# Optimization experiments

Hardware: AMD Instinct MI355X
Metric: run time of the kernel (lower is better)

Reference implementation:

```python
import jax, jax.numpy as jnp
import numpy as np
from jax import lax

NL, HID, DIN, DST, DCONV, DTR = 4, 256, 512, 16, 4, 16  # layers, d_model, expand*d_model, d_state, d_conv, dt_rank
B, H, W = 4, 256, 256


def setup_inputs() -> dict:
    key = jax.random.key(0)
    ks = jax.random.split(key, 8)
    def n(k, s, sc=0.02):
        return jax.random.normal(k, s, dtype=jnp.float32) * sc
    return {
        "x": jax.random.normal(ks[0], (B, 3, H, W), dtype=jnp.float32),
        "conv1_w": n(ks[1], (HID // 2, 3, 3, 3), 0.1), "conv1_b": jnp.zeros((HID // 2,), jnp.float32),
        "gn1_w": jnp.ones((HID // 2,), jnp.float32), "gn1_b": jnp.zeros((HID // 2,), jnp.float32),
        "conv2_w": n(ks[2], (HID, HID // 2, 3, 3), 0.05), "conv2_b": jnp.zeros((HID,), jnp.float32),
        "gn2_w": jnp.ones((HID,), jnp.float32), "gn2_b": jnp.zeros((HID,), jnp.float32),
        "ln_w": jnp.ones((NL, HID), jnp.float32), "ln_b": jnp.zeros((NL, HID), jnp.float32),
        "in_proj_w": n(ks[3], (NL, 2 * DIN, HID)),
        "conv1d_w": n(ks[4], (NL, DIN, 1, DCONV), 0.1), "conv1d_b": jnp.zeros((NL, DIN), jnp.float32),
        "x_proj_w": n(ks[5], (NL, DTR + 2 * DST, DIN)),
        "dt_proj_w": n(ks[6], (NL, DIN, DTR), 0.1),
        "dt_proj_b": jnp.full((NL, DIN), -4.6, dtype=jnp.float32),  # softplus(-4.6) ~ 0.01
        "A_log": jnp.broadcast_to(jnp.log(jnp.arange(1, DST + 1, dtype=jnp.float32)), (NL, DIN, DST)) + jnp.zeros((NL, DIN, DST), jnp.float32),
        "D": jnp.ones((NL, DIN), jnp.float32),
        "out_proj_w": n(ks[7], (NL, HID, DIN)),
    }


def conv2d_s2(x, w, b):
    y = lax.conv_general_dilated(x, w, (2, 2), [(1, 1), (1, 1)],
                                 dimension_numbers=('NCHW', 'OIHW', 'NCHW'))
    return y + b[None, :, None, None]


def group_norm(x, w, b, groups=8, eps=1e-5):
    Bb, C, Hh, Ww = x.shape
    xg = x.reshape(Bb, groups, C // groups, Hh, Ww)
    m = xg.mean((2, 3, 4), keepdims=True)
    v = xg.var((2, 3, 4), keepdims=True)
    xg = (xg - m) * lax.rsqrt(v + eps)
    return xg.reshape(Bb, C, Hh, Ww) * w[None, :, None, None] + b[None, :, None, None]


def layer_norm(x, w, b, eps=1e-5):
    m = x.mean(-1, keepdims=True)
    v = x.var(-1, keepdims=True)
    return (x - m) * lax.rsqrt(v + eps) * w + b


def mamba(x, ipw, cw, cb, xpw, dpw, dpb, A_log, Dp, opw):
    # x: [B, L, HID]
    Bb, L, _ = x.shape
    xz = jnp.einsum('bld,ed->ble', x, ipw)           # [B, L, 2*DIN]
    xc, z = jnp.split(xz, 2, axis=-1)
    # depthwise causal conv1d over L
    u = xc.transpose(0, 2, 1)                        # [B, DIN, L]
    u = lax.conv_general_dilated(u, cw, (1,), [(DCONV - 1, 0)],
                                 dimension_numbers=('NCH', 'OIH', 'NCH'),
                                 feature_group_count=DIN)
    xc = jax.nn.silu(u + cb[None, :, None]).transpose(0, 2, 1)  # [B, L, DIN]
    x_dbl = jnp.einsum('bld,ed->ble', xc, xpw)       # [B, L, DTR+2*DST]
    dt, Bm, Cm = jnp.split(x_dbl, [DTR, DTR + DST], axis=-1)
    delta = jax.nn.softplus(jnp.einsum('blr,dr->bld', dt, dpw) + dpb)  # [B, L, DIN]
    A = -jnp.exp(A_log)                              # [DIN, DST]
    dA = jnp.exp(jnp.einsum('bld,dn->bldn', delta, A))
    dBu = jnp.einsum('bld,bln,bld->bldn', delta, Bm, xc)

    def step(h, inp):
        dA_t, dBu_t, C_t = inp
        h = dA_t * h + dBu_t                         # [B, DIN, DST]
        return h, jnp.einsum('bdn,bn->bd', h, C_t)

    h0 = jnp.zeros((Bb, DIN, DST), x.dtype)
    _, ys = lax.scan(step, h0, (dA.transpose(1, 0, 2, 3), dBu.transpose(1, 0, 2, 3), Cm.transpose(1, 0, 2)))
    y = ys.transpose(1, 0, 2) + xc * Dp              # [B, L, DIN]
    y = y * jax.nn.silu(z)
    return jnp.einsum('bld,ed->ble', y, opw)         # [B, L, HID]


def reference(x, conv1_w, conv1_b, gn1_w, gn1_b, conv2_w, conv2_b, gn2_w, gn2_b,
              ln_w, ln_b, in_proj_w, conv1d_w, conv1d_b, x_proj_w, dt_proj_w,
              dt_proj_b, A_log, D, out_proj_w):
    y = jax.nn.silu(group_norm(conv2d_s2(x, conv1_w, conv1_b), gn1_w, gn1_b))
    y = jax.nn.silu(group_norm(conv2d_s2(y, conv2_w, conv2_b), gn2_w, gn2_b))
    Bb, C, h, w = y.shape
    s = y.reshape(Bb, C, h * w).transpose(0, 2, 1)   # b (h w) c
    for i in range(NL):
        s = s + mamba(layer_norm(s, ln_w[i], ln_b[i]), in_proj_w[i], conv1d_w[i],
                      conv1d_b[i], x_proj_w[i], dt_proj_w[i], dt_proj_b[i],
                      A_log[i], D[i], out_proj_w[i])
    return (s, h, w)
```

## Files before the change

### kernel.cpp

```cpp
#include <hip/hip_runtime.h>
#include <math.h>

#define BB 4
#define C1 128
#define H1 128
#define W1 128
#define C2 256
#define H2 64
#define W2 64
#define LSEQ 4096
#define HID 256
#define DIN 512
#define DST 16
#define DTR 16
#define NL 4
#define NCHUNK 64
#define LCH 64

typedef unsigned short u16;
using short8 = __attribute__((ext_vector_type(8))) short;
using f32x4  = __attribute__((ext_vector_type(4))) float;
using f32x2  = __attribute__((ext_vector_type(2))) float;

static __device__ __forceinline__ float dsilu(float x){
    return x / (1.0f + __expf(-x));
}
static __device__ __forceinline__ u16 f2bf(float f){
    unsigned u = __float_as_uint(f);
    u += 0x7FFF + ((u >> 16) & 1);
    return (u16)(u >> 16);
}
static __device__ __forceinline__ float bf2f(u16 v){
    return __uint_as_float(((unsigned)v) << 16);
}

#define GLL16(g, l) __builtin_amdgcn_global_load_lds( \
    (const __attribute__((address_space(1))) void*)(g), \
    (__attribute__((address_space(3))) void*)(l), 16, 0, 0)
#define GLL4(g, l) __builtin_amdgcn_global_load_lds( \
    (const __attribute__((address_space(1))) void*)(g), \
    (__attribute__((address_space(3))) void*)(l), 4, 0, 0)

#define VMW(n) asm volatile("s_waitcnt vmcnt(" #n ")" ::: "memory")

static __device__ __forceinline__ void blockbar(){
    asm volatile("" ::: "memory");
    __builtin_amdgcn_s_barrier();
    asm volatile("" ::: "memory");
}

__global__ void f2bf_kernel(const float* __restrict__ src, u16* __restrict__ dst){
    int idx = blockIdx.x * 256 + threadIdx.x;
    dst[idx] = f2bf(src[idx]);
}
__global__ void wdt_prep_kernel(const float* __restrict__ xpw, const float* __restrict__ dpw,
                                u16* __restrict__ wcomb){
    int idx = blockIdx.x * 256 + threadIdx.x;
    int k = idx & 511;
    int n = (idx >> 9) % 640;
    int layer = idx / (640*512);
    u16 val = 0;
    if(n < 512){
        const float* dp = dpw + ((long)layer*512 + n)*16;
        const float* xp = xpw + (long)layer*48*512 + k;
        float acc = 0.f;
        #pragma unroll
        for(int r = 0; r < 16; ++r) acc = fmaf(dp[r], xp[(long)r*512], acc);
        val = f2bf(acc);
    } else if(n < 544){
        int row = n - 512 + 16;
        val = f2bf(xpw[((long)layer*48 + row)*512 + k]);
    }
    wcomb[((long)layer*640 + n)*512 + k] = val;
}
__global__ void c2w_prep_kernel(const float* __restrict__ src, u16* __restrict__ dst){
    int idx = blockIdx.x * 256 + threadIdx.x;
    int ci = idx & 127, p = (idx >> 7) % 9, co = idx / (9*128);
    int kh = p / 3, kw = p - 3*kh;
    dst[idx] = f2bf(src[((co*128 + ci)*3 + kh)*3 + kw]);
}
__global__ void xt_border_kernel(unsigned* __restrict__ xt){
    int idx = blockIdx.x * 256 + threadIdx.x;
    int c2 = idx & 63;
    int cell = (idx >> 6) % 516;
    int b = idx / (516*64);
    int ih, iw;
    if(cell < 130){ ih = 0; iw = cell; }
    else if(cell < 260){ ih = 129; iw = cell - 130; }
    else if(cell < 388){ iw = 0; ih = cell - 259; }
    else { iw = 129; ih = cell - 387; }
    xt[((long)(b*130 + ih)*130 + iw)*64 + c2] = 0;
}

__global__ __launch_bounds__(256) void conv1_kernel(
        const float* __restrict__ x, const float* __restrict__ w,
        const float* __restrict__ bias, float* __restrict__ y){
    __shared__ float xs[9][260];
    int oh = blockIdx.x, b = blockIdx.y;
    int tid = threadIdx.x;
    #pragma unroll
    for(int r = 0; r < 9; ++r){
        int ci = r / 3, kh = r - 3*ci;
        int ih = 2*oh - 1 + kh;
        float v = 0.f;
        if(ih >= 0) v = x[((b*3 + ci)*256 + ih)*256 + tid];
        xs[r][tid + 1] = v;
        if(tid == 0) xs[r][0] = 0.f;
    }
    __syncthreads();
    int co = tid >> 1, h = tid & 1;
    float wr[27];
    #pragma unroll
    for(int j = 0; j < 27; ++j) wr[j] = w[co*27 + j];
    float bz = bias[co];
    long obase = ((long)((b*128 + co)*128 + oh))*128 + h*64;
    #pragma unroll 4
    for(int i = 0; i < 64; ++i){
        int iw0 = 2*(h*64 + i);
        float acc = bz;
        #pragma unroll
        for(int r = 0; r < 9; ++r){
            acc = fmaf(xs[r][iw0+0], wr[r*3+0], acc);
            acc = fmaf(xs[r][iw0+1], wr[r*3+1], acc);
            acc = fmaf(xs[r][iw0+2], wr[r*3+2], acc);
        }
        y[obase + i] = acc;
    }
}

__global__ void zero_stats_kernel(float* __restrict__ stats){
    stats[threadIdx.x] = 0.0f;
}

__global__ void gn_stats_kernel(const float* __restrict__ x, float* __restrict__ stats,
                                int elems_per_group){
    const int EPB = 16384;
    long base = (long)blockIdx.x * EPB;
    int g = (int)(base / elems_per_group);
    float s = 0.f, ss = 0.f;
    for(int j = threadIdx.x; j < EPB; j += 256){
        float v = x[base + j];
        s += v; ss += v*v;
    }
    #pragma unroll
    for(int off = 32; off; off >>= 1){
        s  += __shfl_down(s,  off);
        ss += __shfl_down(ss, off);
    }
    __shared__ float ls[4], lss[4];
    int wid = threadIdx.x >> 6, lane = threadIdx.x & 63;
    if(lane == 0){ ls[wid] = s; lss[wid] = ss; }
    __syncthreads();
    if(threadIdx.x == 0){
        atomicAdd(&stats[g],      ls[0]+ls[1]+ls[2]+ls[3]);
        atomicAdd(&stats[32+g], lss[0]+lss[1]+lss[2]+lss[3]);
    }
}

__global__ void gn1_transform_kernel(const float* __restrict__ y1, const float* __restrict__ stats,
                                     const float* __restrict__ w, const float* __restrict__ bias,
                                     u16* __restrict__ xt){
    __shared__ float tile[32][33];
    int b = blockIdx.z >> 7, ih = blockIdx.z & 127;
    int c0 = blockIdx.y * 32, w0 = blockIdx.x * 32;
    int tx = threadIdx.x, ty = threadIdx.y;
    const float cnt = 16.f * 128.f * 128.f;
    #pragma unroll
    for(int i = 0; i < 4; ++i){
        int ci = c0 + ty + i*8;
        int g = b*8 + (ci >> 4);
        float mean = stats[g] / cnt;
        float var  = stats[32+g] / cnt - mean*mean;
        float rstd = rsqrtf(var + 1e-5f);
        float v = y1[(((long)(b*C1 + ci))*H1 + ih)*W1 + w0 + tx];
        tile[ty + i*8][tx] = dsilu((v - mean) * rstd * w[ci] + bias[ci]);
    }
    __syncthreads();
    #pragma unroll
    for(int i = 0; i < 4; ++i){
        int iwl = ty + i*8;
        xt[((long)(b*130 + ih + 1)*130 + (w0 + iwl + 1))*128 + c0 + tx] = f2bf(tile[tx][iwl]);
    }
}

__global__ __launch_bounds__(256) void conv2gemm_bf16_kernel(
        const u16* __restrict__ xt, const u16* __restrict__ w2,
        const float* __restrict__ bias, float* __restrict__ y2t){
    __shared__ u16 Asm[3][64*32];
    __shared__ u16 Bsm[3][128*32];
    int m0 = blockIdx.x * 64, n0 = blockIdx.y * 128;
    int tid = threadIdx.x;
    long abase;
    {
        int r = tid >> 2;
        int kq = ((tid & 3) ^ ((r >> 1) & 3)) * 8;
        int m = m0 + r;
        int b = m >> 12, oh = (m >> 6) & 63, ow = m & 63;
        abase = ((long)(b*130 + 2*oh)*130 + 2*ow)*128 + kq;
    }
    int lda = tid*8;
    const u16* bbase[2]; int ldb[2];
    #pragma unroll
    for(int it = 0; it < 2; ++it){
        int c = it*256 + tid;
        int r = c >> 2;
        int kq = ((c & 3) ^ ((r >> 1) & 3)) * 8;
        bbase[it] = w2 + (long)(n0 + r)*1152 + kq;
        ldb[it] = c*8;
    }
    int wave = tid >> 6, lane = tid & 63;
    int wr = wave >> 1, wc = wave & 1;
    int lm = lane & 15, lq = lane >> 4;
    int swq = (lq ^ ((lm >> 1) & 3)) * 8;
    f32x4 acc[2][4] = {};
    #pragma unroll
    for(int pt = 0; pt < 2; ++pt){
        int p = pt >> 2, cs = pt & 3;
        int kh = p / 3, kw = p - 3*kh;
        int ao = (kh*130 + kw)*128 + cs*32;
        GLL16(xt + abase + ao, &Asm[pt][lda]);
        #pragma unroll
        for(int it = 0; it < 2; ++it)
            GLL16(bbase[it] + pt*32, &Bsm[pt][ldb[it]]);
    }
    for(int kk = 0; kk < 36; ++kk){
        int cur = kk % 3;
        if(kk + 2 < 36){
            int k2 = kk + 2;
            int nxt = (kk + 2) % 3;
            int p = k2 >> 2, cs = k2 & 3;
            int kh = p / 3, kw = p - 3*kh;
            int ao = (kh*130 + kw)*128 + cs*32;
            GLL16(xt + abase + ao, &Asm[nxt][lda]);
            #pragma unroll
            for(int it = 0; it < 2; ++it)
                GLL16(bbase[it] + k2*32, &Bsm[nxt][ldb[it]]);
            VMW(6);
        } else if(kk + 1 < 36){
            VMW(3);
        } else {
            VMW(0);
        }
        blockbar();
        short8 af[2], bf[4];
        #pragma unroll
        for(int i = 0; i < 2; ++i)
            af[i] = *(const short8*)&Asm[cur][(wr*32 + i*16 + lm)*32 + swq];
        #pragma unroll
        for(int j = 0; j < 4; ++j)
            bf[j] = *(const short8*)&Bsm[cur][(wc*64 + j*16 + lm)*32 + swq];
        #pragma unroll
        for(int i = 0; i < 2; ++i)
            #pragma unroll
            for(int j = 0; j < 4; ++j)
                acc[i][j] = __builtin_amdgcn_mfma_f32_16x16x32_bf16(af[i], bf[j], acc[i][j], 0, 0, 0);
        __builtin_amdgcn_sched_barrier(0);
        blockbar();
    }
    #pragma unroll
    for(int i = 0; i < 2; ++i){
        long row = m0 + wr*32 + i*16 + lq*4;
        #pragma unroll
        for(int j = 0; j < 4; ++j){
            int col = n0 + wc*64 + j*16 + lm;
            float bz = bias[col];
            #pragma unroll
            for(int r = 0; r < 4; ++r)
                y2t[(row + r)*256L + col] = acc[i][j][r] + bz;
        }
    }
}

__global__ void gn2t_stats_kernel(const float* __restrict__ y2t, float* __restrict__ stats){
    int b = blockIdx.y;
    long row0 = (long)b*LSEQ + blockIdx.x*64;
    int c = threadIdx.x;
    float s = 0.f, ss = 0.f;
    for(int r = 0; r < 64; ++r){
        float v = y2t[(row0 + r)*C2 + c];
        s += v; ss += v*v;
    }
    #pragma unroll
    for(int off = 16; off; off >>= 1){
        s  += __shfl_down(s,  off);
        ss += __shfl_down(ss, off);
    }
    if((c & 31) == 0){
        int g = b*8 + (c >> 5);
        atomicAdd(&stats[g], s);
        atomicAdd(&stats[32+g], ss);
    }
}

__global__ void gn2t_apply_ln_kernel(const float* __restrict__ y2t, const float* __restrict__ stats,
                                     const float* __restrict__ gw, const float* __restrict__ gb,
                                     const float* __restrict__ lw, const float* __restrict__ lb,
                                     float* __restrict__ s, u16* __restrict__ xln){
    long row = blockIdx.x;
    int c = threadIdx.x;
    int b = (int)(row >> 12);
    int g = b*8 + (c >> 5);
    const float cnt = 32.f * (float)LSEQ;
    float mean = stats[g] / cnt;
    float var  = stats[32+g] / cnt - mean*mean;
    float rstd = rsqrtf(var + 1e-5f);
    float v = dsilu((y2t[row*HID + c] - mean) * rstd * gw[c] + gb[c]);
    s[row*HID + c] = v;
    float sm = v, sq = v*v;
    #pragma unroll
    for(int off = 32; off; off >>= 1){
        sm += __shfl_down(sm, off);
        sq += __shfl_down(sq, off);
    }
    __shared__ float pa[4], pb[4], res[2];
    int wid = c >> 6, lane = c & 63;
    if(lane == 0){ pa[wid] = sm; pb[wid] = sq; }
    __syncthreads();
    if(c == 0){
        float t  = pa[0]+pa[1]+pa[2]+pa[3];
        float tt = pb[0]+pb[1]+pb[2]+pb[3];
        float m2 = t / 256.f;
        float v2 = tt / 256.f - m2*m2;
        res[0] = m2; res[1] = rsqrtf(v2 + 1e-5f);
    }
    __syncthreads();
    xln[row*HID + c] = f2bf((v - res[0]) * res[1] * lw[c] + lb[c]);
}

__global__ __launch_bounds__(256) void gemm_bf16_kernel(
        const u16* __restrict__ A, const u16* __restrict__ B, void* __restrict__ Cv,
        int K, int Nact, int ldc, int mode){
    __shared__ u16 Asm[3][128*32];
    __shared__ u16 Bsm[3][128*32];
    int m0 = blockIdx.x * 128, n0 = blockIdx.y * 128;
    int tid = threadIdx.x;
    int wave = tid >> 6, lane = tid & 63;
    int wr = wave >> 1, wc = wave & 1;
    int lm = lane & 15, lq = lane >> 4;
    int swq = (lq ^ ((lm >> 1) & 3)) * 8;
    const u16* ag[2]; const u16* bg[2]; int ldst[2];
    #pragma unroll
    for(int it = 0; it < 2; ++it){
        int c = it*256 + tid;
        int r = c >> 2;
        int kq = ((c & 3) ^ ((r >> 1) & 3)) * 8;
        ag[it] = A + (long)(m0 + r)*K + kq;
        bg[it] = B + (long)(n0 + r)*K + kq;
        ldst[it] = c*8;
    }
    f32x4 acc[4][4] = {};
    int nk = K >> 5;
    #pragma unroll
    for(int pt = 0; pt < 2; ++pt){
        int ko = pt << 5;
        #pragma unroll
        for(int it = 0; it < 2; ++it){
            GLL16(ag[it] + ko, &Asm[pt][ldst[it]]);
            GLL16(bg[it] + ko, &Bsm[pt][ldst[it]]);
        }
    }
    for(int kt = 0; kt < nk; ++kt){
        int cur = kt % 3;
        if(kt + 2 < nk){
            int nxt = (kt + 2) % 3;
            int ko = (kt + 2) << 5;
            #pragma unroll
            for(int it = 0; it < 2; ++it){
                GLL16(ag[it] + ko, &Asm[nxt][ldst[it]]);
                GLL16(bg[it] + ko, &Bsm[nxt][ldst[it]]);
            }
            VMW(8);
        } else if(kt + 1 < nk){
            VMW(4);
        } else {
            VMW(0);
        }
        blockbar();
        short8 af[4], bf[4];
        #pragma unroll
        for(int i = 0; i < 4; ++i){
            af[i] = *(const short8*)&Asm[cur][(wr*64 + i*16 + lm)*32 + swq];
            bf[i] = *(const short8*)&Bsm[cur][(wc*64 + i*16 + lm)*32 + swq];
        }
        #pragma unroll
        for(int i = 0; i < 4; ++i)
            #pragma unroll
            for(int j = 0; j < 4; ++j)
                acc[i][j] = __builtin_amdgcn_mfma_f32_16x16x32_bf16(af[i], bf[j], acc[i][j], 0, 0, 0);
        __builtin_amdgcn_sched_barrier(0);
        blockbar();
    }
    #pragma unroll
    for(int i = 0; i < 4; ++i){
        long row = m0 + wr*64 + i*16 + lq*4;
        #pragma unroll
        for(int j = 0; j < 4; ++j){
            int col = n0 + wc*64 + j*16 + lm;
            if(col < Nact){
                #pragma unroll
                for(int r = 0; r < 4; ++r){
                    long idx = (row + r)*(long)ldc + col;
                    if(mode == 2) ((u16*)Cv)[idx] = f2bf(acc[i][j][r]);
                    else          ((float*)Cv)[idx] = acc[i][j][r];
                }
            }
        }
    }
}

__global__ __launch_bounds__(256) void gemm_dtbc_kernel(
        const u16* __restrict__ A, const u16* __restrict__ B,
        const float* __restrict__ dpb, u16* __restrict__ dv,
        float* __restrict__ xdbl32){
    __shared__ u16 Asm[3][128*32];
    __shared__ u16 Bsm[3][128*32];
    int m0 = blockIdx.x * 128, n0 = blockIdx.y * 128;
    int tid = threadIdx.x;
    int wave = tid >> 6, lane = tid & 63;
    int wr = wave >> 1, wc = wave & 1;
    int lm = lane & 15, lq = lane >> 4;
    int swq = (lq ^ ((lm >> 1) & 3)) * 8;
    const u16* ag[2]; const u16* bg[2]; int ldst[2];
    #pragma unroll
    for(int it = 0; it < 2; ++it){
        int c = it*256 + tid;
        int r = c >> 2;
        int kq = ((c & 3) ^ ((r >> 1) & 3)) * 8;
        ag[it] = A + (long)(m0 + r)*512 + kq;
        bg[it] = B + (long)(n0 + r)*512 + kq;
        ldst[it] = c*8;
    }
    f32x4 acc[4][4] = {};
    #pragma unroll
    for(int pt = 0; pt < 2; ++pt){
        int ko = pt << 5;
        #pragma unroll
        for(int it = 0; it < 2; ++it){
            GLL16(ag[it] + ko, &Asm[pt][ldst[it]]);
            GLL16(bg[it] + ko, &Bsm[pt][ldst[it]]);
        }
    }
    for(int kt = 0; kt < 16; ++kt){
        int cur = kt % 3;
        if(kt + 2 < 16){
            int nxt = (kt + 2) % 3;
            int ko = (kt + 2) << 5;
            #pragma unroll
            for(int it = 0; it < 2; ++it){
                GLL16(ag[it] + ko, &Asm[nxt][ldst[it]]);
                GLL16(bg[it] + ko, &Bsm[nxt][ldst[it]]);
            }
            VMW(8);
        } else if(kt + 1 < 16){
            VMW(4);
        } else {
            VMW(0);
        }
        blockbar();
        short8 af[4], bf[4];
        #pragma unroll
        for(int i = 0; i < 4; ++i){
            af[i] = *(const short8*)&Asm[cur][(wr*64 + i*16 + lm)*32 + swq];
            bf[i] = *(const short8*)&Bsm[cur][(wc*64 + i*16 + lm)*32 + swq];
        }
        #pragma unroll
        for(int i = 0; i < 4; ++i)
            #pragma unroll
            for(int j = 0; j < 4; ++j)
                acc[i][j] = __builtin_amdgcn_mfma_f32_16x16x32_bf16(af[i], bf[j], acc[i][j], 0, 0, 0);
        __builtin_amdgcn_sched_barrier(0);
        blockbar();
    }
    if(n0 < 512){
        #pragma unroll
        for(int i = 0; i < 4; ++i){
            long row = m0 + wr*64 + i*16 + lq*4;
            #pragma unroll
            for(int j = 0; j < 4; ++j){
                int col = n0 + wc*64 + j*16 + lm;
                float bz = dpb[col];
                #pragma unroll
                for(int r = 0; r < 4; ++r){
                    float v = acc[i][j][r] + bz;
                    v = (v > 20.f) ? v : __logf(1.f + __expf(v));
                    dv[(row + r)*512L + col] = f2bf(v);
                }
            }
        }
    } else {
        #pragma unroll
        for(int i = 0; i < 4; ++i){
            long row = m0 + wr*64 + i*16 + lq*4;
            #pragma unroll
            for(int j = 0; j < 4; ++j){
                int lcol = wc*64 + j*16 + lm;
                if(lcol < 32){
                    #pragma unroll
                    for(int r = 0; r < 4; ++r)
                        xdbl32[(row + r)*32L + lcol] = acc[i][j][r];
                }
            }
        }
    }
}

__global__ __launch_bounds__(256) void gemm_out_ln_kernel(
        const u16* __restrict__ A, const u16* __restrict__ B,
        float* __restrict__ s, u16* __restrict__ xln,
        const float* __restrict__ lw, const float* __restrict__ lb){
    __shared__ u16 Asm[3][32*32];
    __shared__ u16 Bsm[3][256*32];
    __shared__ float lnred[2][2][16][2];
    int m0 = blockIdx.x * 32;
    int tid = threadIdx.x;
    int wave = tid >> 6, lane = tid & 63;
    int wr = wave >> 1, wc = wave & 1;
    int lm = lane & 15, lq = lane >> 4;
    int swq = (lq ^ ((lm >> 1) & 3)) * 8;
    const u16* agA[2]; int lda[2];
    #pragma unroll
    for(int it = 0; it < 2; ++it){
        int c = it*256 + tid;
// ... 47 lines not shown
        blockbar();
    }
    int row0 = m0 + wr*16 + lq*4;
    float psum[4] = {0.f,0.f,0.f,0.f}, psq[4] = {0.f,0.f,0.f,0.f};
    #pragma unroll
    for(int j = 0; j < 8; ++j){
        int col = wc*128 + j*16 + lm;
        #pragma unroll
        for(int r = 0; r < 4; ++r){
            long idx = (long)(row0 + r)*HID + col;
            float v = s[idx] + acc[j][r];
            acc[j][r] = v;
            s[idx] = v;
            psum[r] += v; psq[r] += v*v;
        }
    }
    #pragma unroll
    for(int mask = 1; mask <= 8; mask <<= 1){
        #pragma unroll
        for(int r = 0; r < 4; ++r){
            psum[r] += __shfl_xor(psum[r], mask);
            psq[r]  += __shfl_xor(psq[r],  mask);
        }
    }
    if(lm == 0){
        #pragma unroll
        for(int r = 0; r < 4; ++r){
            lnred[wr][wc][lq*4 + r][0] = psum[r];
            lnred[wr][wc][lq*4 + r][1] = psq[r];
        }
    }
    __syncthreads();
    float mean[4], rstd[4];
    #pragma unroll
    for(int r = 0; r < 4; ++r){
        float t  = lnred[wr][0][lq*4 + r][0] + lnred[wr][1][lq*4 + r][0];
        float tt = lnred[wr][0][lq*4 + r][1] + lnred[wr][1][lq*4 + r][1];
        mean[r] = t * (1.f/256.f);
        float var = tt * (1.f/256.f) - mean[r]*mean[r];
        rstd[r] = rsqrtf(var + 1e-5f);
    }
    #pragma unroll
    for(int j = 0; j < 8; ++j){
        int col = wc*128 + j*16 + lm;
        float wv = lw[col], bv = lb[col];
        #pragma unroll
        for(int r = 0; r < 4; ++r){
            long idx = (long)(row0 + r)*HID + col;
            xln[idx] = f2bf((acc[j][r] - mean[r]) * rstd[r] * wv + bv);
        }
    }
}

__global__ void conv1d_silu_kernel(const u16* __restrict__ xz, const float* __restrict__ w,
                                   const float* __restrict__ bias, u16* __restrict__ xcv){
    int idx = blockIdx.x * 256 + threadIdx.x;
    int e = idx * 8;
    int d0 = e & 511;
    long m = e >> 9;
    int l = (int)(m & 4095);
    short8 xrow[4];
    const u16* xp = xz + m*(2*DIN) + d0;
    #pragma unroll
    for(int j = 0; j < 4; ++j){
        int t = l - 3 + j;
        if(t >= 0) xrow[j] = *(const short8*)(xp + (long)(j-3)*(2*DIN));
        else       xrow[j] = (short8){0,0,0,0,0,0,0,0};
    }
    float wv[8][4];
    #pragma unroll
    for(int k = 0; k < 8; k += 2){
        float4 a = *(const float4*)(w + (d0+k)*4);
        float4 b = *(const float4*)(w + (d0+k+1)*4);
        wv[k][0]=a.x; wv[k][1]=a.y; wv[k][2]=a.z; wv[k][3]=a.w;
        wv[k+1][0]=b.x; wv[k+1][1]=b.y; wv[k+1][2]=b.z; wv[k+1][3]=b.w;
    }
    float bz[8];
    {
        float4 a = *(const float4*)(bias + d0);
        float4 b = *(const float4*)(bias + d0 + 4);
        bz[0]=a.x; bz[1]=a.y; bz[2]=a.z; bz[3]=a.w;
        bz[4]=b.x; bz[5]=b.y; bz[6]=b.z; bz[7]=b.w;
    }
    short8 out;
    #pragma unroll
    for(int k = 0; k < 8; ++k){
        float acc = bz[k];
        #pragma unroll
        for(int j = 0; j < 4; ++j)
            acc = fmaf(bf2f((u16)xrow[j][k]), wv[k][j], acc);
        out[k] = (short)f2bf(dsilu(acc));
    }
    *(short8*)(xcv + m*DIN + d0) = out;
}

__global__ __launch_bounds__(256) void scan1_kernel(
        const u16* __restrict__ xcvb, const u16* __restrict__ dvin,
        const float* __restrict__ xdbl32, const float* __restrict__ Alog,
        float* __restrict__ aprod, float* __restrict__ hend){
    int d = blockIdx.y * 256 + threadIdx.x;
    int c = blockIdx.x;
    int b = blockIdx.z;
    __shared__ float bm[LCH][16];
    {
        int t = threadIdx.x >> 4, n = threadIdx.x & 15;
        #pragma unroll
        for(int it = 0; it < 4; ++it){
            long p = ((long)(b*LSEQ + c*LCH + t + it*16))*32;
            bm[t + it*16][n] = xdbl32[p + n];
        }
    }
    __syncthreads();
    float An[16];
    #pragma unroll
    for(int n = 0; n < 16; ++n)
        An[n] = -__expf(Alog[d*16 + n]);
    float An0 = An[0];
    bool structural = true;
    #pragma unroll
    for(int n = 0; n < 16; ++n)
        structural = structural && (fabsf(An[n] - (float)(n+1)*An0) <= 1e-3f*(float)(n+1));
    long base = ((long)(b*LSEQ + c*LCH))*DIN + d;
    long ob = (((long)(b*NCHUNK + c))*DIN + d)*16;
    if(structural){
        f32x2 h2[8];
        #pragma unroll
        for(int i = 0; i < 8; ++i) h2[i] = (f32x2){0.f, 0.f};
        float sumdv = 0.f;
        float xv_n = bf2f(xcvb[base]);
        float dv_n = bf2f(dvin[base]);
        for(int t = 0; t < LCH; ++t){
            float xv = xv_n, dv = dv_n;
            if(t + 1 < LCH){
                xv_n = bf2f(xcvb[base + (long)(t+1)*DIN]);
                dv_n = bf2f(dvin[base + (long)(t+1)*DIN]);
            }
            sumdv += dv;
            float db = dv * xv;
            float r1 = __expf(dv * An0);
            float r2 = r1 * r1;
            f32x2 rr = {r2, r2};
            f32x2 e2[8];
            e2[0] = (f32x2){r1, r2};
            #pragma unroll
            for(int i = 1; i < 8; ++i) e2[i] = e2[i-1] * rr;
            f32x2 db2 = {db, db};
            const f32x2* b2 = (const f32x2*)&bm[t][0];
            #pragma unroll
            for(int i = 0; i < 8; ++i) h2[i] = e2[i]*h2[i] + db2*b2[i];
        }
        float R = __expf(An0 * sumdv);
        float Rp = R;
        const float* hp = (const float*)h2;
        #pragma unroll
        for(int n = 0; n < 16; ++n){
            aprod[ob+n] = Rp; Rp *= R;
            hend[ob+n] = hp[n];
        }
    } else {
        float h[16], ap[16];
        #pragma unroll
        for(int n = 0; n < 16; ++n){ h[n] = 0.f; ap[n] = 1.f; }
        for(int t = 0; t < LCH; ++t){
            float dv = bf2f(dvin[base + (long)t*DIN]);
            float db = dv * bf2f(xcvb[base + (long)t*DIN]);
            #pragma unroll
            for(int n = 0; n < 16; ++n){
                float e = __expf(dv * An[n]);
                ap[n] *= e;
                h[n] = fmaf(e, h[n], db * bm[t][n]);
            }
        }
        #pragma unroll
        for(int n = 0; n < 16; ++n){ aprod[ob+n] = ap[n]; hend[ob+n] = h[n]; }
    }
}

__global__ void scan2_kernel(const float* __restrict__ aprod, const float* __restrict__ hend,
                             float* __restrict__ hinit){
    int idx = blockIdx.x * 256 + threadIdx.x;
    int n = idx & 15, d = (idx >> 4) & 511, b = idx >> 13;
    const long stride = (long)DIN * 16;
    long p0 = (((long)(b*NCHUNK))*DIN + d)*16 + n;
    float h = 0.f;
    for(int c = 0; c < NCHUNK; c += 8){
        float a[8], e[8];
        #pragma unroll
        for(int j = 0; j < 8; ++j){
            long p = p0 + (long)(c + j)*stride;
            a[j] = aprod[p]; e[j] = hend[p];
        }
        #pragma unroll
        for(int j = 0; j < 8; ++j){
            hinit[p0 + (long)(c + j)*stride] = h;
            h = fmaf(a[j], h, e[j]);
        }
    }
}

__global__ __launch_bounds__(256) void scan3_kernel(
        const u16* __restrict__ xcvb, const u16* __restrict__ dvin,
        const float* __restrict__ xdbl32, const float* __restrict__ Alog,
        const float* __restrict__ hinit, const float* __restrict__ Dp,
        const u16* __restrict__ xz, u16* __restrict__ yout){
    int d = blockIdx.y * 256 + threadIdx.x;
    int c = blockIdx.x;
    int b = blockIdx.z;
    __shared__ float bm[LCH][16], cm[LCH][16];
    {
        int t = threadIdx.x >> 4, n = threadIdx.x & 15;
        #pragma unroll
        for(int it = 0; it < 4; ++it){
            long p = ((long)(b*LSEQ + c*LCH + t + it*16))*32;
            bm[t + it*16][n] = xdbl32[p + n];
            cm[t + it*16][n] = xdbl32[p + 16 + n];
        }
    }
    __syncthreads();
    float An[16];
    long hb = (((long)(b*NCHUNK + c))*DIN + d)*16;
    #pragma unroll
    for(int n = 0; n < 16; ++n)
        An[n] = -__expf(Alog[d*16 + n]);
    float An0 = An[0];
    bool structural = true;
    #pragma unroll
    for(int n = 0; n < 16; ++n)
        structural = structural && (fabsf(An[n] - (float)(n+1)*An0) <= 1e-3f*(float)(n+1));
    float Dv = Dp[d];
    long base  = ((long)(b*LSEQ + c*LCH))*DIN + d;
    long zbase = ((long)(b*LSEQ + c*LCH))*(2*DIN) + DIN + d;
    if(structural){
        f32x2 h2[8];
        {
            const f32x2* hi = (const f32x2*)&hinit[hb];
            #pragma unroll
            for(int i = 0; i < 8; ++i) h2[i] = hi[i];
        }
        float xv_n = bf2f(xcvb[base]);
        float z_n  = bf2f(xz[zbase]);
        float dv_n = bf2f(dvin[base]);
        for(int t = 0; t < LCH; ++t){
            float xv = xv_n, z = z_n, dv = dv_n;
            if(t + 1 < LCH){
                xv_n = bf2f(xcvb[base + (long)(t+1)*DIN]);
                z_n  = bf2f(xz[zbase + (long)(t+1)*(2*DIN)]);
                dv_n = bf2f(dvin[base + (long)(t+1)*DIN]);
            }
            float db = dv * xv;
            float r1 = __expf(dv * An0);
            float r2 = r1 * r1;
            f32x2 rr = {r2, r2};
            f32x2 e2[8];
            e2[0] = (f32x2){r1, r2};
            #pragma unroll
            for(int i = 1; i < 8; ++i) e2[i] = e2[i-1] * rr;
            f32x2 db2 = {db, db};
            const f32x2* b2 = (const f32x2*)&bm[t][0];
            const f32x2* c2 = (const f32x2*)&cm[t][0];
            f32x2 y2 = {0.f, 0.f};
            #pragma unroll
            for(int i = 0; i < 8; ++i){
                h2[i] = e2[i]*h2[i] + db2*b2[i];
                y2 = y2 + h2[i]*c2[i];
            }
            float y = y2[0] + y2[1];
            y = fmaf(xv, Dv, y);
            yout[base + (long)t*DIN] = f2bf(y * dsilu(z));
        }
    } else {
        float h[16];
        #pragma unroll
        for(int n = 0; n < 16; ++n) h[n] = hinit[hb + n];
// ... 9 lines not shown
                y = fmaf(h[n], cm[t][n], y);
            }
            y = fmaf(xv, Dv, y);
            float z = bf2f(xz[zbase + (long)t*(2*DIN)]);
            yout[base + (long)t*DIN] = f2bf(y * dsilu(z));
        }
    }
}

__global__ void copyout_kernel(const float* __restrict__ s, float* __restrict__ out, int out_size){
    int idx = blockIdx.x * 256 + threadIdx.x;
    if(idx >= out_size) return;
    out[idx] = (idx < BB*LSEQ*HID) ? s[idx] : 64.0f;
}

extern "C" void kernel_launch(void* const* d_in, const int* in_sizes, int n_in,
                              void* d_out, int out_size, void* d_ws, size_t ws_size,
                              hipStream_t stream){
    const float* x        = (const float*)d_in[0];
    const float* conv1_w  = (const float*)d_in[1];
    const float* conv1_b  = (const float*)d_in[2];
    const float* gn1_w    = (const float*)d_in[3];
    const float* gn1_b    = (const float*)d_in[4];
    const float* conv2_w  = (const float*)d_in[5];
    const float* conv2_b  = (const float*)d_in[6];
    const float* gn2_w    = (const float*)d_in[7];
    const float* gn2_b    = (const float*)d_in[8];
    const float* ln_w     = (const float*)d_in[9];
    const float* ln_b     = (const float*)d_in[10];
    const float* in_proj  = (const float*)d_in[11];
    const float* c1d_w    = (const float*)d_in[12];
    const float* c1d_b    = (const float*)d_in[13];
    const float* x_proj   = (const float*)d_in[14];
    const float* dt_w     = (const float*)d_in[15];
    const float* dt_b     = (const float*)d_in[16];
    const float* A_log    = (const float*)d_in[17];
    const float* Dvec     = (const float*)d_in[18];
    const float* out_proj = (const float*)d_in[19];

    float* ws = (float*)d_ws;
    float* s      = ws;
    u16*   xz_bf  = (u16*)(ws + 4194304);
    float* y1     = ws + 4194304;
    u16*   xt     = (u16*)(ws + 12582912);
    u16*   xcv_bf = (u16*)(ws + 16909312);
    float* y2t    = ws + 16909312;
    u16*   xln_bf = (u16*)(ws + 21103616);
    float* xdbl   = ws + 23200768;
    float* aprod  = ws + 23987200;
    float* hendb  = ws + 28181504;
    u16*   y_bf   = (u16*)aprod;
    float* hinit  = ws + 32375808;
    float* stats  = ws + 36570112;
    u16*   ipw_bf = (u16*)(ws + 36570176);
    u16*   opw_bf = ipw_bf + 1048576;
    u16*   c2w_bf = opw_bf + 524288;
    u16*   dv_bf  = (u16*)(ws + 37635200);
    u16*   wcomb  = (u16*)(ws + 41829504);

    f2bf_kernel<<<4096, 256, 0, stream>>>(in_proj, ipw_bf);
    f2bf_kernel<<<2048, 256, 0, stream>>>(out_proj, opw_bf);
    c2w_prep_kernel<<<1152, 256, 0, stream>>>(conv2_w, c2w_bf);
    wdt_prep_kernel<<<5120, 256, 0, stream>>>(x_proj, dt_w, wcomb);

    conv1_kernel<<<dim3(128,4), 256, 0, stream>>>(x, conv1_w, conv1_b, y1);
    zero_stats_kernel<<<1, 64, 0, stream>>>(stats);
    gn_stats_kernel<<<512, 256, 0, stream>>>(y1, stats, 16*H1*W1);
    xt_border_kernel<<<516, 256, 0, stream>>>((unsigned*)xt);
    gn1_transform_kernel<<<dim3(4,4,512), dim3(32,8), 0, stream>>>(y1, stats, gn1_w, gn1_b, xt);
    conv2gemm_bf16_kernel<<<dim3(256,2), 256, 0, stream>>>(xt, c2w_bf, conv2_b, y2t);
    zero_stats_kernel<<<1, 64, 0, stream>>>(stats);
    gn2t_stats_kernel<<<dim3(64,4), 256, 0, stream>>>(y2t, stats);
    gn2t_apply_ln_kernel<<<16384, 256, 0, stream>>>(y2t, stats, gn2_w, gn2_b,
                                                    ln_w, ln_b, s, xln_bf);

    for(int layer = 0; layer < NL; ++layer){
        const float* cw  = c1d_w + (long)layer*DIN*4;
        const float* cb  = c1d_b + (long)layer*DIN;
        const float* dpb = dt_b  + (long)layer*DIN;
        const float* Al  = A_log + (long)layer*DIN*DST;
        const float* Dl  = Dvec  + (long)layer*DIN;
        int lnext = (layer + 1) & 3;

        gemm_bf16_kernel<<<dim3(128,8), 256, 0, stream>>>(
            xln_bf, ipw_bf + (long)layer*1024*256, xz_bf, HID, 2*DIN, 2*DIN, 2);
        conv1d_silu_kernel<<<4096, 256, 0, stream>>>(xz_bf, cw, cb, xcv_bf);
        gemm_dtbc_kernel<<<dim3(128,5), 256, 0, stream>>>(
            xcv_bf, wcomb + (long)layer*640*512, dpb, dv_bf, xdbl);
        scan1_kernel<<<dim3(NCHUNK,2,BB), 256, 0, stream>>>(
            xcv_bf, dv_bf, xdbl, Al, aprod, hendb);
        scan2_kernel<<<128, 256, 0, stream>>>(aprod, hendb, hinit);
        scan3_kernel<<<dim3(NCHUNK,2,BB), 256, 0, stream>>>(
            xcv_bf, dv_bf, xdbl, Al, hinit, Dl, xz_bf, y_bf);
        gemm_out_ln_kernel<<<512, 256, 0, stream>>>(
            y_bf, opw_bf + (long)layer*256*512, s, xln_bf,
            ln_w + lnext*HID, ln_b + lnext*HID);
    }

    copyout_kernel<<<(out_size + 255)/256, 256, 0, stream>>>(s, (float*)d_out, out_size);
}
```

Before: 783.7 us.

## Fuse prep kernels, GN stats into convs, conv1d into in_proj GEMM

Merges the weight-conversion, border-zeroing and stats-zeroing kernels into one prep launch. It folds GroupNorm statistics accumulation into the conv1 and conv2 GEMM epilogues and moves GN2 stats to a separate stats region. It fuses the depthwise causal conv1d plus SiLU into the in_proj GEMM epilogue, recomputing the three halo rows with a scalar dot product. It also skips MFMA work on padded dtbc columns and transposes the scan chunk-state layout for coalesced scan2 access. This removes several launches and full passes over intermediates, at the cost of extra halo recompute and more atomics.

```diff
diff --git a/kernel.cpp b/kernel.cpp
--- a/kernel.cpp
+++ b/kernel.cpp
@@ -49,52 +49,74 @@
     asm volatile("" ::: "memory");
 }
 
-__global__ void f2bf_kernel(const float* __restrict__ src, u16* __restrict__ dst){
-    int idx = blockIdx.x * 256 + threadIdx.x;
-    dst[idx] = f2bf(src[idx]);
-}
-__global__ void wdt_prep_kernel(const float* __restrict__ xpw, const float* __restrict__ dpw,
-                                u16* __restrict__ wcomb){
-    int idx = blockIdx.x * 256 + threadIdx.x;
-    int k = idx & 511;
-    int n = (idx >> 9) % 640;
-    int layer = idx / (640*512);
-    u16 val = 0;
-    if(n < 512){
-        const float* dp = dpw + ((long)layer*512 + n)*16;
-        const float* xp = xpw + (long)layer*48*512 + k;
-        float acc = 0.f;
-        #pragma unroll
-        for(int r = 0; r < 16; ++r) acc = fmaf(dp[r], xp[(long)r*512], acc);
-        val = f2bf(acc);
-    } else if(n < 544){
-        int row = n - 512 + 16;
-        val = f2bf(xpw[((long)layer*48 + row)*512 + k]);
-    }
-    wcomb[((long)layer*640 + n)*512 + k] = val;
-}
-__global__ void c2w_prep_kernel(const float* __restrict__ src, u16* __restrict__ dst){
-    int idx = blockIdx.x * 256 + threadIdx.x;
-    int ci = idx & 127, p = (idx >> 7) % 9, co = idx / (9*128);
-    int kh = p / 3, kw = p - 3*kh;
-    dst[idx] = f2bf(src[((co*128 + ci)*3 + kh)*3 + kw]);
-}
-__global__ void xt_border_kernel(unsigned* __restrict__ xt){
-    int idx = blockIdx.x * 256 + threadIdx.x;
-    int c2 = idx & 63;
-    int cell = (idx >> 6) % 516;
-    int b = idx / (516*64);
-    int ih, iw;
-    if(cell < 130){ ih = 0; iw = cell; }
-    else if(cell < 260){ ih = 129; iw = cell - 130; }
-    else if(cell < 388){ iw = 0; ih = cell - 259; }
-    else { iw = 129; ih = cell - 387; }
-    xt[((long)(b*130 + ih)*130 + iw)*64 + c2] = 0;
+__global__ void prep_kernel(const float* __restrict__ in_proj, const float* __restrict__ out_proj,
+                            const float* __restrict__ conv2_w, const float* __restrict__ xpw,
+                            const float* __restrict__ dpw,
+                            u16* __restrict__ ipw_bf, u16* __restrict__ opw_bf,
+                            u16* __restrict__ c2w_bf, u16* __restrict__ wcomb,
+                            unsigned* __restrict__ xt, float* __restrict__ stats){
+    int bx = blockIdx.x, tid = threadIdx.x;
+    if(bx < 4096){
+        int idx = bx*256 + tid;
+        ipw_bf[idx] = f2bf(in_proj[idx]);
+        return;
+    }
+    bx -= 4096;
+    if(bx < 2048){
+        int idx = bx*256 + tid;
+        opw_bf[idx] = f2bf(out_proj[idx]);
+        return;
+    }
+    bx -= 2048;
+    if(bx < 1152){
+        int idx = bx*256 + tid;
+        int ci = idx & 127, p = (idx >> 7) % 9, co = idx / (9*128);
+        int kh = p / 3, kw = p - 3*kh;
+        c2w_bf[idx] = f2bf(conv2_w[((co*128 + ci)*3 + kh)*3 + kw]);
+        return;
+    }
+    bx -= 1152;
+    if(bx < 5120){
+        int idx = bx*256 + tid;
+        int k = idx & 511;
+        int n = (idx >> 9) % 640;
+        int layer = idx / (640*512);
+        u16 val = 0;
+        if(n < 512){
+            const float* dp = dpw + ((long)layer*512 + n)*16;
+            const float* xp = xpw + (long)layer*48*512 + k;
+            float acc = 0.f;
+            #pragma unroll
+            for(int r = 0; r < 16; ++r) acc = fmaf(dp[r], xp[(long)r*512], acc);
+            val = f2bf(acc);
+        } else if(n < 544){
+            int row = n - 512 + 16;
+            val = f2bf(xpw[((long)layer*48 + row)*512 + k]);
+        }
+        wcomb[((long)layer*640 + n)*512 + k] = val;
+        return;
+    }
+    bx -= 5120;
+    if(bx < 516){
+        int idx = bx*256 + tid;
+        int c2 = idx & 63;
+        int cell = (idx >> 6) % 516;
+        int b = idx / (516*64);
+        int ih, iw;
+        if(cell < 130){ ih = 0; iw = cell; }
+        else if(cell < 260){ ih = 129; iw = cell - 130; }
+        else if(cell < 388){ iw = 0; ih = cell - 259; }
+        else { iw = 129; ih = cell - 387; }
+        xt[((long)(b*130 + ih)*130 + iw)*64 + c2] = 0;
+        return;
+    }
+    if(tid < 128) stats[tid] = 0.f;
 }
 
 __global__ __launch_bounds__(256) void conv1_kernel(
         const float* __restrict__ x, const float* __restrict__ w,
-        const float* __restrict__ bias, float* __restrict__ y){
+        const float* __restrict__ bias, float* __restrict__ y,
+        float* __restrict__ stats){
     __shared__ float xs[9][260];
     int oh = blockIdx.x, b = blockIdx.y;
     int tid = threadIdx.x;
@@ -114,6 +136,7 @@
     for(int j = 0; j < 27; ++j) wr[j] = w[co*27 + j];
     float bz = bias[co];
     long obase = ((long)((b*128 + co)*128 + oh))*128 + h*64;
+    float s = 0.f, ss = 0.f;
     #pragma unroll 4
     for(int i = 0; i < 64; ++i){
         int iw0 = 2*(h*64 + i);
@@ -125,35 +148,17 @@
             acc = fmaf(xs[r][iw0+2], wr[r*3+2], acc);
         }
         y[obase + i] = acc;
-    }
-}
-
-__global__ void zero_stats_kernel(float* __restrict__ stats){
-    stats[threadIdx.x] = 0.0f;
-}
-
-__global__ void gn_stats_kernel(const float* __restrict__ x, float* __restrict__ stats,
-                                int elems_per_group){
-    const int EPB = 16384;
-    long base = (long)blockIdx.x * EPB;
-    int g = (int)(base / elems_per_group);
-    float s = 0.f, ss = 0.f;
-    for(int j = threadIdx.x; j < EPB; j += 256){
-        float v = x[base + j];
-        s += v; ss += v*v;
-    }
-    #pragma unroll
-    for(int off = 32; off; off >>= 1){
+        s += acc; ss += acc*acc;
+    }
+    #pragma unroll
+    for(int off = 16; off; off >>= 1){
         s  += __shfl_down(s,  off);
         ss += __shfl_down(ss, off);
     }
-    __shared__ float ls[4], lss[4];
-    int wid = threadIdx.x >> 6, lane = threadIdx.x & 63;
-    if(lane == 0){ ls[wid] = s; lss[wid] = ss; }
-    __syncthreads();
-    if(threadIdx.x == 0){
-        atomicAdd(&stats[g],      ls[0]+ls[1]+ls[2]+ls[3]);
-        atomicAdd(&stats[32+g], lss[0]+lss[1]+lss[2]+lss[3]);
+    if((tid & 31) == 0){
+        int g = b*8 + (tid >> 5);
+        atomicAdd(&stats[g], s);
+        atomicAdd(&stats[32 + g], ss);
     }
 }
 
@@ -185,7 +190,8 @@
 
 __global__ __launch_bounds__(256) void conv2gemm_bf16_kernel(
         const u16* __restrict__ xt, const u16* __restrict__ w2,
-        const float* __restrict__ bias, float* __restrict__ y2t){
+        const float* __restrict__ bias, float* __restrict__ y2t,
+        float* __restrict__ stats){
     __shared__ u16 Asm[3][64*32];
     __shared__ u16 Bsm[3][128*32];
     int m0 = blockIdx.x * 64, n0 = blockIdx.y * 128;
@@ -257,6 +263,7 @@
         __builtin_amdgcn_sched_barrier(0);
         blockbar();
     }
+    float gs0 = 0.f, gss0 = 0.f, gs1 = 0.f, gss1 = 0.f;
     #pragma unroll
     for(int i = 0; i < 2; ++i){
         long row = m0 + wr*32 + i*16 + lq*4;
@@ -265,30 +272,25 @@
             int col = n0 + wc*64 + j*16 + lm;
             float bz = bias[col];
             #pragma unroll
-            for(int r = 0; r < 4; ++r)
-                y2t[(row + r)*256L + col] = acc[i][j][r] + bz;
-        }
-    }
-}
-
-__global__ void gn2t_stats_kernel(const float* __restrict__ y2t, float* __restrict__ stats){
-    int b = blockIdx.y;
-    long row0 = (long)b*LSEQ + blockIdx.x*64;
-    int c = threadIdx.x;
-    float s = 0.f, ss = 0.f;
-    for(int r = 0; r < 64; ++r){
-        float v = y2t[(row0 + r)*C2 + c];
-        s += v; ss += v*v;
-    }
-    #pragma unroll
-    for(int off = 16; off; off >>= 1){
-        s  += __shfl_down(s,  off);
-        ss += __shfl_down(ss, off);
-    }
-    if((c & 31) == 0){
-        int g = b*8 + (c >> 5);
-        atomicAdd(&stats[g], s);
-        atomicAdd(&stats[32+g], ss);
+            for(int r = 0; r < 4; ++r){
+                float v = acc[i][j][r] + bz;
+                y2t[(row + r)*256L + col] = v;
+                if(j < 2){ gs0 += v; gss0 += v*v; } else { gs1 += v; gss1 += v*v; }
+            }
+        }
+    }
+    #pragma unroll
+    for(int off = 32; off; off >>= 1){
+        gs0 += __shfl_down(gs0, off); gss0 += __shfl_down(gss0, off);
+        gs1 += __shfl_down(gs1, off); gss1 += __shfl_down(gss1, off);
+    }
+    if(lane == 0){
+        int b = m0 >> 12;
+        int gb = b*8 + (n0 >> 5) + wc*2;
+        atomicAdd(&stats[64 + gb],     gs0);
+        atomicAdd(&stats[96 + gb],     gss0);
+        atomicAdd(&stats[64 + gb + 1], gs1);
+        atomicAdd(&stats[96 + gb + 1], gss1);
     }
 }
 
@@ -301,8 +303,8 @@
     int b = (int)(row >> 12);
     int g = b*8 + (c >> 5);
     const float cnt = 32.f * (float)LSEQ;
-    float mean = stats[g] / cnt;
-    float var  = stats[32+g] / cnt - mean*mean;
+    float mean = stats[64+g] / cnt;
+    float var  = stats[96+g] / cnt - mean*mean;
     float rstd = rsqrtf(var + 1e-5f);
     float v = dsilu((y2t[row*HID + c] - mean) * rstd * gw[c] + gb[c]);
     s[row*HID + c] = v;
@@ -327,11 +329,13 @@
     xln[row*HID + c] = f2bf((v - res[0]) * res[1] * lw[c] + lb[c]);
 }
 
-__global__ __launch_bounds__(256) void gemm_bf16_kernel(
-        const u16* __restrict__ A, const u16* __restrict__ B, void* __restrict__ Cv,
-        int K, int Nact, int ldc, int mode){
-    __shared__ u16 Asm[3][128*32];
-    __shared__ u16 Bsm[3][128*32];
+__global__ __launch_bounds__(256) void gemm_inproj_conv_kernel(
+        const u16* __restrict__ A, const u16* __restrict__ B,
+        u16* __restrict__ xz, u16* __restrict__ xcv,
+        const float* __restrict__ cw, const float* __restrict__ cb){
+    __shared__ u16 smem[24576];
+    u16* Abuf = smem;
+    u16* Bbuf = smem + 12288;
     int m0 = blockIdx.x * 128, n0 = blockIdx.y * 128;
     int tid = threadIdx.x;
     int wave = tid >> 6, lane = tid & 63;
@@ -344,33 +348,32 @@
         int c = it*256 + tid;
         int r = c >> 2;
         int kq = ((c & 3) ^ ((r >> 1) & 3)) * 8;
-        ag[it] = A + (long)(m0 + r)*K + kq;
-        bg[it] = B + (long)(n0 + r)*K + kq;
+        ag[it] = A + (long)(m0 + r)*256 + kq;
+        bg[it] = B + (long)(n0 + r)*256 + kq;
         ldst[it] = c*8;
     }
     f32x4 acc[4][4] = {};
-    int nk = K >> 5;
     #pragma unroll
     for(int pt = 0; pt < 2; ++pt){
         int ko = pt << 5;
         #pragma unroll
         for(int it = 0; it < 2; ++it){
-            GLL16(ag[it] + ko, &Asm[pt][ldst[it]]);
-            GLL16(bg[it] + ko, &Bsm[pt][ldst[it]]);
-        }
-    }
-    for(int kt = 0; kt < nk; ++kt){
+            GLL16(ag[it] + ko, &Abuf[pt*4096 + ldst[it]]);
+            GLL16(bg[it] + ko, &Bbuf[pt*4096 + ldst[it]]);
+        }
+    }
+    for(int kt = 0; kt < 8; ++kt){
         int cur = kt % 3;
-        if(kt + 2 < nk){
+        if(kt + 2 < 8){
             int nxt = (kt + 2) % 3;
             int ko = (kt + 2) << 5;
             #pragma unroll
             for(int it = 0; it < 2; ++it){
-                GLL16(ag[it] + ko, &Asm[nxt][ldst[it]]);
-                GLL16(bg[it] + ko, &Bsm[nxt][ldst[it]]);
+                GLL16(ag[it] + ko, &Abuf[nxt*4096 + ldst[it]]);
+                GLL16(bg[it] + ko, &Bbuf[nxt*4096 + ldst[it]]);
             }
             VMW(8);
-        } else if(kt + 1 < nk){
+        } else if(kt + 1 < 8){
             VMW(4);
         } else {
             VMW(0);
@@ -379,8 +382,8 @@
         short8 af[4], bf[4];
         #pragma unroll
         for(int i = 0; i < 4; ++i){
-            af[i] = *(const short8*)&Asm[cur][(wr*64 + i*16 + lm)*32 + swq];
-            bf[i] = *(const short8*)&Bsm[cur][(wc*64 + i*16 + lm)*32 + swq];
+            af[i] = *(const short8*)&Abuf[cur*4096 + (wr*64 + i*16 + lm)*32 + swq];
+            bf[i] = *(const short8*)&Bbuf[cur*4096 + (wc*64 + i*16 + lm)*32 + swq];
         }
         #pragma unroll
         for(int i = 0; i < 4; ++i)
@@ -390,20 +393,70 @@
         __builtin_amdgcn_sched_barrier(0);
         blockbar();
     }
+    if(n0 >= 512){
+        #pragma unroll
+        for(int i = 0; i < 4; ++i){
+            long row = m0 + wr*64 + i*16 + lq*4;
+            #pragma unroll
+            for(int j = 0; j < 4; ++j){
+                int col = n0 + wc*64 + j*16 + lm;
+                #pragma unroll
+                for(int r = 0; r < 4; ++r)
+                    xz[(row + r)*1024L + col] = f2bf(acc[i][j][r]);
+            }
+        }
+        return;
+    }
+    u16* xcs = smem;
+    bool first = ((m0 & 4095) == 0);
+    for(int jj = tid; jj < 384; jj += 256){
+        int hr = jj >> 7, cc = jj & 127;
+        u16 val = 0;
+        if(!first){
+            const u16* ar = A + (long)(m0 - 3 + hr)*256;
+            const u16* br = B + (long)(n0 + cc)*256;
+            float a2 = 0.f;
+            #pragma unroll 4
+            for(int k = 0; k < 256; k += 8){
+                short8 av = *(const short8*)(ar + k);
+                short8 bv = *(const short8*)(br + k);
+                #pragma unroll
+                for(int q = 0; q < 8; ++q)
+                    a2 = fmaf(bf2f((u16)av[q]), bf2f((u16)bv[q]), a2);
+            }
+            val = f2bf(a2);
+        }
+        xcs[hr*128 + cc] = val;
+    }
     #pragma unroll
     for(int i = 0; i < 4; ++i){
-        long row = m0 + wr*64 + i*16 + lq*4;
+        int rl = wr*64 + i*16 + lq*4;
         #pragma unroll
         for(int j = 0; j < 4; ++j){
-            int col = n0 + wc*64 + j*16 + lm;
-            if(col < Nact){
-                #pragma unroll
-                for(int r = 0; r < 4; ++r){
-                    long idx = (row + r)*(long)ldc + col;
-                    if(mode == 2) ((u16*)Cv)[idx] = f2bf(acc[i][j][r]);
-                    else          ((float*)Cv)[idx] = acc[i][j][r];
-                }
-            }
+            int cl = wc*64 + j*16 + lm;
+            #pragma unroll
+            for(int r = 0; r < 4; ++r)
+                xcs[(3 + rl + r)*128 + cl] = f2bf(acc[i][j][r]);
+        }
+    }
+    __syncthreads();
+    {
+        int c = tid & 127, h = tid >> 7;
+        float4 w4 = *(const float4*)(cw + (n0 + c)*4);
+        float bz = cb[n0 + c];
+        int r0 = h*64;
+        float v0 = bf2f(xcs[(r0+0)*128 + c]);
+        float v1 = bf2f(xcs[(r0+1)*128 + c]);
+        float v2 = bf2f(xcs[(r0+2)*128 + c]);
+        long gbase = (long)(m0 + r0)*512 + n0 + c;
+        for(int i2 = 0; i2 < 64; ++i2){
+            float v3 = bf2f(xcs[(r0+3+i2)*128 + c]);
+            float a2 = fmaf(v0, w4.x, bz);
+            a2 = fmaf(v1, w4.y, a2);
+            a2 = fmaf(v2, w4.z, a2);
+            a2 = fmaf(v3, w4.w, a2);
+            xcv[gbase + (long)i2*512] = f2bf(dsilu(a2));
+            v0 = v1; v1 = v2; v2 = v3;
         }
     }
 }
@@ -420,6 +473,7 @@
     int wr = wave >> 1, wc = wave & 1;
     int lm = lane & 15, lq = lane >> 4;
     int swq = (lq ^ ((lm >> 1) & 3)) * 8;
+    int jlim = (n0 < 512) ? 4 : ((wc == 0) ? 2 : 0);
     const u16* ag[2]; const u16* bg[2]; int ldst[2];
     #pragma unroll
     for(int it = 0; it < 2; ++it){
@@ -457,17 +511,16 @@
             VMW(0);
         }
         blockbar();
-        short8 af[4], bf[4];
-        #pragma unroll
-        for(int i = 0; i < 4; ++i){
+        short8 af[4];
+        #pragma unroll
+        for(int i = 0; i < 4; ++i)
             af[i] = *(const short8*)&Asm[cur][(wr*64 + i*16 + lm)*32 + swq];
-            bf[i] = *(const short8*)&Bsm[cur][(wc*64 + i*16 + lm)*32 + swq];
-        }
-        #pragma unroll
-        for(int i = 0; i < 4; ++i)
-            #pragma unroll
-            for(int j = 0; j < 4; ++j)
-                acc[i][j] = __builtin_amdgcn_mfma_f32_16x16x32_bf16(af[i], bf[j], acc[i][j], 0, 0, 0);
+        for(int j = 0; j < jlim; ++j){
+            short8 bf = *(const short8*)&Bsm[cur][(wc*64 + j*16 + lm)*32 + swq];
+            #pragma unroll
+            for(int i = 0; i < 4; ++i)
+                acc[i][j] = __builtin_amdgcn_mfma_f32_16x16x32_bf16(af[i], bf, acc[i][j], 0, 0, 0);
+        }
         __builtin_amdgcn_sched_barrier(0);
         blockbar();
     }
@@ -621,48 +674,6 @@
     }
 }
 
-__global__ void conv1d_silu_kernel(const u16* __restrict__ xz, const float* __restrict__ w,
-                                   const float* __restrict__ bias, u16* __restrict__ xcv){
-    int idx = blockIdx.x * 256 + threadIdx.x;
-    int e = idx * 8;
-    int d0 = e & 511;
-    long m = e >> 9;
-    int l = (int)(m & 4095);
-    short8 xrow[4];
-    const u16* xp = xz + m*(2*DIN) + d0;
-    #pragma unroll
-    for(int j = 0; j < 4; ++j){
-        int t = l - 3 + j;
-        if(t >= 0) xrow[j] = *(const short8*)(xp + (long)(j-3)*(2*DIN));
-        else       xrow[j] = (short8){0,0,0,0,0,0,0,0};
-    }
-    float wv[8][4];
-    #pragma unroll
-    for(int k = 0; k < 8; k += 2){
-        float4 a = *(const float4*)(w + (d0+k)*4);
-        float4 b = *(const float4*)(w + (d0+k+1)*4);
-        wv[k][0]=a.x; wv[k][1]=a.y; wv[k][2]=a.z; wv[k][3]=a.w;
-        wv[k+1][0]=b.x; wv[k+1][1]=b.y; wv[k+1][2]=b.z; wv[k+1][3]=b.w;
-    }
-    float bz[8];
-    {
-        float4 a = *(const float4*)(bias + d0);
-        float4 b = *(const float4*)(bias + d0 + 4);
-        bz[0]=a.x; bz[1]=a.y; bz[2]=a.z; bz[3]=a.w;
-        bz[4]=b.x; bz[5]=b.y; bz[6]=b.z; bz[7]=b.w;
-    }
-    short8 out;
-    #pragma unroll
-    for(int k = 0; k < 8; ++k){
-        float acc = bz[k];
-        #pragma unroll
-        for(int j = 0; j < 4; ++j)
-            acc = fmaf(bf2f((u16)xrow[j][k]), wv[k][j], acc);
-        out[k] = (short)f2bf(dsilu(acc));
-    }
-    *(short8*)(xcv + m*DIN + d0) = out;
-}
-
 __global__ __launch_bounds__(256) void scan1_kernel(
         const u16* __restrict__ xcvb, const u16* __restrict__ dvin,
         const float* __restrict__ xdbl32, const float* __restrict__ Alog,
@@ -690,7 +701,7 @@
     for(int n = 0; n < 16; ++n)
         structural = structural && (fabsf(An[n] - (float)(n+1)*An0) <= 1e-3f*(float)(n+1));
     long base = ((long)(b*LSEQ + c*LCH))*DIN + d;
-    long ob = (((long)(b*NCHUNK + c))*DIN + d)*16;
+    long ob = (long)c*32768 + ((long)b*DIN + d)*16;
     if(structural){
         f32x2 h2[8];
         #pragma unroll
@@ -747,21 +758,19 @@
 
 __global__ void scan2_kernel(const float* __restrict__ aprod, const float* __restrict__ hend,
                              float* __restrict__ hinit){
-    int idx = blockIdx.x * 256 + threadIdx.x;
-    int n = idx & 15, d = (idx >> 4) & 511, b = idx >> 13;
-    const long stride = (long)DIN * 16;
-    long p0 = (((long)(b*NCHUNK))*DIN + d)*16 + n;
+    int gtid = blockIdx.x * 256 + threadIdx.x;
+    const long S = 32768;
     float h = 0.f;
-    for(int c = 0; c < NCHUNK; c += 8){
+    for(int cc = 0; cc < NCHUNK; cc += 8){
         float a[8], e[8];
         #pragma unroll
         for(int j = 0; j < 8; ++j){
-            long p = p0 + (long)(c + j)*stride;
+            long p = (long)(cc + j)*S + gtid;
             a[j] = aprod[p]; e[j] = hend[p];
         }
         #pragma unroll
         for(int j = 0; j < 8; ++j){
-            hinit[p0 + (long)(c + j)*stride] = h;
+            hinit[(long)(cc + j)*S + gtid] = h;
             h = fmaf(a[j], h, e[j]);
         }
     }
@@ -787,7 +796,7 @@
     }
     __syncthreads();
     float An[16];
-    long hb = (((long)(b*NCHUNK + c))*DIN + d)*16;
+    long hb = (long)c*32768 + ((long)b*DIN + d)*16;
     #pragma unroll
     for(int n = 0; n < 16; ++n)
         An[n] = -__expf(Alog[d*16 + n]);
@@ -903,25 +912,19 @@
     u16*   y_bf   = (u16*)aprod;
     float* hinit  = ws + 32375808;
     float* stats  = ws + 36570112;
-    u16*   ipw_bf = (u16*)(ws + 36570176);
+    u16*   ipw_bf = (u16*)(ws + 36570240);
     u16*   opw_bf = ipw_bf + 1048576;
     u16*   c2w_bf = opw_bf + 524288;
-    u16*   dv_bf  = (u16*)(ws + 37635200);
-    u16*   wcomb  = (u16*)(ws + 41829504);
-
-    f2bf_kernel<<<4096, 256, 0, stream>>>(in_proj, ipw_bf);
-    f2bf_kernel<<<2048, 256, 0, stream>>>(out_proj, opw_bf);
-    c2w_prep_kernel<<<1152, 256, 0, stream>>>(conv2_w, c2w_bf);
-    wdt_prep_kernel<<<5120, 256, 0, stream>>>(x_proj, dt_w, wcomb);
-
-    conv1_kernel<<<dim3(128,4), 256, 0, stream>>>(x, conv1_w, conv1_b, y1);
-    zero_stats_kernel<<<1, 64, 0, stream>>>(stats);
-    gn_stats_kernel<<<512, 256, 0, stream>>>(y1, stats, 16*H1*W1);
-    xt_border_kernel<<<516, 256, 0, stream>>>((unsigned*)xt);
+    u16*   dv_bf  = (u16*)(ws + 37635264);
+    u16*   wcomb  = (u16*)(ws + 41829568);
+
+    prep_kernel<<<12933, 256, 0, stream>>>(in_proj, out_proj, conv2_w, x_proj, dt_w,
+                                           ipw_bf, opw_bf, c2w_bf, wcomb,
+                                           (unsigned*)xt, stats);
+
+    conv1_kernel<<<dim3(128,4), 256, 0, stream>>>(x, conv1_w, conv1_b, y1, stats);
     gn1_transform_kernel<<<dim3(4,4,512), dim3(32,8), 0, stream>>>(y1, stats, gn1_w, gn1_b, xt);
-    conv2gemm_bf16_kernel<<<dim3(256,2), 256, 0, stream>>>(xt, c2w_bf, conv2_b, y2t);
-    zero_stats_kernel<<<1, 64, 0, stream>>>(stats);
-    gn2t_stats_kernel<<<dim3(64,4), 256, 0, stream>>>(y2t, stats);
+    conv2gemm_bf16_kernel<<<dim3(256,2), 256, 0, stream>>>(xt, c2w_bf, conv2_b, y2t, stats);
     gn2t_apply_ln_kernel<<<16384, 256, 0, stream>>>(y2t, stats, gn2_w, gn2_b,
                                                     ln_w, ln_b, s, xln_bf);
 
@@ -933,9 +936,8 @@
         const float* Dl  = Dvec  + (long)layer*DIN;
         int lnext = (layer + 1) & 3;
 
-        gemm_bf16_kernel<<<dim3(128,8), 256, 0, stream>>>(
-            xln_bf, ipw_bf + (long)layer*1024*256, xz_bf, HID, 2*DIN, 2*DIN, 2);
-        conv1d_silu_kernel<<<4096, 256, 0, stream>>>(xz_bf, cw, cb, xcv_bf);
+        gemm_inproj_conv_kernel<<<dim3(128,8), 256, 0, stream>>>(
+            xln_bf, ipw_bf + (long)layer*1024*256, xz_bf, xcv_bf, cw, cb);
         gemm_dtbc_kernel<<<dim3(128,5), 256, 0, stream>>>(
             xcv_bf, wcomb + (long)layer*640*512, dpb, dv_bf, xdbl);
         scan1_kernel<<<dim3(NCHUNK,2,BB), 256, 0, stream>>>(
```

Result: slower. 1.388 ms (+77.2%).
